# Kernel tuning notes

Measured on AMD Instinct MI355X. Metric: run time of the kernel, lower is better.

Reference implementation:

```python
import jax, jax.numpy as jnp
import numpy as np

DELTA_VAR = 0.5
DELTA_DIST = 1.5
VAR_WEIGHT = 1.0
DIST_WEIGHT = 1.0
REG_WEIGHT = 0.001
K = 16  # number of clusters (labels are in [0, K))


def setup_inputs() -> dict:
    key = jax.random.key(0)
    k1, k2 = jax.random.split(key)
    data = jax.random.normal(k1, (32, 512, 1024), dtype=jnp.float32)
    labels = jax.random.randint(k2, (512, 1024), 0, K, dtype=jnp.int32)
    return {"data": data, "labels": labels}


def reference(data, labels):
    D = data.shape[0]
    pts = data.reshape(D, -1).T          # [N, D] per-pixel embeddings
    lab = labels.reshape(-1)             # [N]

    # Per-cluster size and mean (center). All K clusters are present.
    counts = jax.ops.segment_sum(jnp.ones_like(lab, dtype=pts.dtype), lab,
                                 num_segments=K)          # [K]
    sums = jax.ops.segment_sum(pts, lab, num_segments=K)  # [K, D]
    centers = sums / counts[:, None]                      # [K, D]

    # Variance term: sum over all points of hinge(||center - x|| - dv)^2 / K
    diff = centers[lab] - pts                             # [N, D]
    dist = jnp.sqrt(jnp.sum(diff * diff, axis=-1))        # [N]
    var_term = jnp.sum(jnp.maximum(dist - DELTA_VAR, 0.0) ** 2) / K

    # Distance term: ordered pairs i != j of hinge(2*dd - ||ci - cj||)^2
    cd = centers[:, None, :] - centers[None, :, :]        # [K, K, D]
    sq = jnp.sum(cd * cd, axis=-1)                        # [K, K]
    eye = jnp.eye(K, dtype=bool)
    pd = jnp.sqrt(jnp.where(eye, 1.0, sq))                # safe sqrt on diag
    hinge = jnp.where(eye, 0.0, jnp.maximum(2.0 * DELTA_DIST - pd, 0.0) ** 2)
    dist_term = jnp.sum(hinge) / (K * (K - 1))

    # Regularization term: mean center norm
    reg_term = jnp.sum(jnp.sqrt(jnp.sum(centers * centers, axis=-1))) / K

    return VAR_WEIGHT * var_term + DIST_WEIGHT * dist_term + REG_WEIGHT * reg_term
```

## Files before the change

### kernel.cpp

```cpp
#include <hip/hip_runtime.h>


constexpr int KC = 16;
constexpr int DD = 32;
constexpr int NN = 512 * 1024;
constexpr int N4 = NN / 4;
constexpr int CHUNKS = 32;
constexpr int GROUPS_PER_CHUNK = N4 / CHUNKS;
constexpr int K1_ITERS = GROUPS_PER_CHUNK / 256;

constexpr int WS_SUMS = 0;
constexpr int WS_CNTS = 8192;
constexpr int WS_CT2  = 8448;
constexpr int WS_ZERO_FLOATS = 8448;

__global__ __launch_bounds__(256) void k1_sums(const float4* __restrict__ data4,
                                               const int4* __restrict__ lab4,
                                               float* __restrict__ ws) {
    const int tid = threadIdx.x;
    const int d = blockIdx.y;
    const bool doCnt = (d == 0);

    __shared__ float acc[256 * 17];
    __shared__ float cnt[256 * 17];
    float* arow = acc + tid * 17;
    float* crow = cnt + tid * 17;
#pragma unroll
    for (int k = 0; k < KC; ++k) arow[k] = 0.f;
    if (doCnt) {
#pragma unroll
        for (int k = 0; k < KC; ++k) crow[k] = 0.f;
    }

    const int base = blockIdx.x * GROUPS_PER_CHUNK + tid;
    const float4* dplane = data4 + (size_t)d * N4;

    for (int it = 0; it < K1_ITERS; ++it) {
        const int g = base + it * 256;
        const float4 v = dplane[g];
        const int4 lb = lab4[g];
        arow[lb.x] += v.x;
        arow[lb.y] += v.y;
        arow[lb.z] += v.z;
        arow[lb.w] += v.w;
        if (doCnt) {
            crow[lb.x] += 1.f;
            crow[lb.y] += 1.f;
            crow[lb.z] += 1.f;
            crow[lb.w] += 1.f;
        }
    }
    __syncthreads();

    const int k = tid >> 4, seg = tid & 15;
    float s = 0.f;
#pragma unroll
    for (int i = 0; i < 16; ++i) s += acc[(seg * 16 + i) * 17 + k];
#pragma unroll
    for (int off = 8; off > 0; off >>= 1) s += __shfl_down(s, off, 16);
    if (seg == 0) atomicAdd(&ws[WS_SUMS + (k * DD + d) * 16], s);
    if (doCnt) {
        float c = 0.f;
#pragma unroll
        for (int i = 0; i < 16; ++i) c += cnt[(seg * 16 + i) * 17 + k];
#pragma unroll
        for (int off = 8; off > 0; off >>= 1) c += __shfl_down(c, off, 16);
        if (seg == 0) atomicAdd(&ws[WS_CNTS + k * 16], c);
    }
}

__global__ __launch_bounds__(256) void k2_centers(float* __restrict__ ws,
                                                  float* __restrict__ out) {
    __shared__ float cent[KC][DD + 1];
    __shared__ float red[256];
    const int tid = threadIdx.x;

    for (int idx = tid; idx < KC * DD; idx += 256) {
        const int k = idx / DD, d = idx % DD;
        const float c = ws[WS_SUMS + idx * 16] / ws[WS_CNTS + k * 16];
        cent[k][d] = c;
        ws[WS_CT2 + d * 32 + k] = c;
        ws[WS_CT2 + d * 32 + 16 + k] = c;
    }
    __syncthreads();

    const int i = tid >> 4, j = tid & 15;
    float sq = 0.f;
#pragma unroll
    for (int d = 0; d < DD; ++d) {
        const float df = cent[i][d] - cent[j][d];
        sq += df * df;
    }
    float val = 0.f;
    if (i != j) {
        const float pd = sqrtf(sq);
        const float t = fmaxf(3.0f - pd, 0.f);
        val = t * t * (1.0f / (KC * (KC - 1)));
    } else {
        float s2 = 0.f;
#pragma unroll
        for (int d = 0; d < DD; ++d) s2 += cent[i][d] * cent[i][d];
        val = sqrtf(s2) * (0.001f / KC);
    }
    red[tid] = val;
    __syncthreads();
    for (int off = 128; off > 0; off >>= 1) {
        if (tid < off) red[tid] += red[tid + off];
        __syncthreads();
    }
    if (tid == 0) out[0] = red[0];
}

__global__ __launch_bounds__(256) void k3_var(const float4* __restrict__ data4,
                                              const int4* __restrict__ lab4,
                                              const float* __restrict__ ws,
                                              float* __restrict__ out) {
    __shared__ float ct2[DD * 32];
    const int tid = threadIdx.x;
    for (int idx = tid; idx < DD * 32; idx += 256) ct2[idx] = ws[WS_CT2 + idx];
    __syncthreads();

    const int g = blockIdx.x * 256 + tid;
    const int4 lb = lab4[g];
    const int dup = (tid & 32) >> 1;
    const int o0 = lb.x + dup, o1 = lb.y + dup, o2 = lb.z + dup, o3 = lb.w + dup;

    float s0 = 0.f, s1 = 0.f, s2 = 0.f, s3 = 0.f;
#pragma unroll 8
    for (int d = 0; d < DD; ++d) {
        const float4 v = data4[(size_t)d * N4 + g];
        const float* ctd = ct2 + d * 32;
        const float d0 = ctd[o0] - v.x; s0 += d0 * d0;
        const float d1 = ctd[o1] - v.y; s1 += d1 * d1;
        const float d2 = ctd[o2] - v.z; s2 += d2 * d2;
        const float d3 = ctd[o3] - v.w; s3 += d3 * d3;
    }
    const float h0 = fmaxf(sqrtf(s0) - 0.5f, 0.f);
    const float h1 = fmaxf(sqrtf(s1) - 0.5f, 0.f);
    const float h2 = fmaxf(sqrtf(s2) - 0.5f, 0.f);
    const float h3 = fmaxf(sqrtf(s3) - 0.5f, 0.f);
    float lsum = h0 * h0 + h1 * h1 + h2 * h2 + h3 * h3;

#pragma unroll
    for (int off = 32; off > 0; off >>= 1) lsum += __shfl_down(lsum, off);
    __shared__ float wred[4];
    if ((tid & 63) == 0) wred[tid >> 6] = lsum;
    __syncthreads();
    if (tid == 0) {
        const float s = wred[0] + wred[1] + wred[2] + wred[3];
        atomicAdd(out, s * (1.0f / KC));
    }
}

extern "C" void kernel_launch(void* const* d_in, const int* in_sizes, int n_in,
                              void* d_out, int out_size, void* d_ws, size_t ws_size,
                              hipStream_t stream) {
    const float4* data4 = (const float4*)d_in[0];
    const int4* lab4 = (const int4*)d_in[1];
    float* out = (float*)d_out;
    float* ws = (float*)d_ws;

    hipMemsetAsync(ws, 0, WS_ZERO_FLOATS * sizeof(float), stream);

    k1_sums<<<dim3(CHUNKS, DD), 256, 0, stream>>>(data4, lab4, ws);
    k2_centers<<<1, 256, 0, stream>>>(ws, out);
    k3_var<<<512, 256, 0, stream>>>(data4, lab4, ws, out);
}
```

Baseline: 122.0 us.

## Drop memset and center kernel by writing per-chunk partials and reducing redundantly

The sums kernel now writes per-chunk partial sums and counts to distinct workspace slots instead of using atomics, so the workspace memset is no longer needed. The separate single-block centers kernel is folded into the variance kernel: every block reduces the partials and computes the centers itself, and block 0 also adds the distance and regularization terms to the output. This cuts two stream operations and their launch gaps, at the cost of each of 512 blocks reading 16K partial floats from L2.

```diff
diff --git a/kernel.cpp b/kernel.cpp
--- a/kernel.cpp
+++ b/kernel.cpp
@@ -9,17 +9,19 @@
 constexpr int GROUPS_PER_CHUNK = N4 / CHUNKS;
 constexpr int K1_ITERS = GROUPS_PER_CHUNK / 256;
 
-constexpr int WS_SUMS = 0;
-constexpr int WS_CNTS = 8192;
-constexpr int WS_CT2  = 8448;
-constexpr int WS_ZERO_FLOATS = 8448;
+constexpr int WS_P  = 0;
+constexpr int WS_CP = 16384;
 
-__global__ __launch_bounds__(256) void k1_sums(const float4* __restrict__ data4,
+__global__ __launch_bounds__(256) void kA_sums(const float4* __restrict__ data4,
                                                const int4* __restrict__ lab4,
-                                               float* __restrict__ ws) {
+                                               float* __restrict__ ws,
+                                               float* __restrict__ out) {
     const int tid = threadIdx.x;
+    const int chunk = blockIdx.x;
     const int d = blockIdx.y;
     const bool doCnt = (d == 0);
+
+    if (chunk == 0 && d == 0 && tid == 0) out[0] = 0.f;
 
     __shared__ float acc[256 * 17];
     __shared__ float cnt[256 * 17];
@@ -32,7 +34,7 @@
         for (int k = 0; k < KC; ++k) crow[k] = 0.f;
     }
 
-    const int base = blockIdx.x * GROUPS_PER_CHUNK + tid;
+    const int base = chunk * GROUPS_PER_CHUNK + tid;
     const float4* dplane = data4 + (size_t)d * N4;
 
     for (int it = 0; it < K1_ITERS; ++it) {
@@ -58,67 +60,86 @@
     for (int i = 0; i < 16; ++i) s += acc[(seg * 16 + i) * 17 + k];
 #pragma unroll
     for (int off = 8; off > 0; off >>= 1) s += __shfl_down(s, off, 16);
-    if (seg == 0) atomicAdd(&ws[WS_SUMS + (k * DD + d) * 16], s);
+    if (seg == 0) ws[WS_P + (k * DD + d) * CHUNKS + chunk] = s;
     if (doCnt) {
         float c = 0.f;
 #pragma unroll
         for (int i = 0; i < 16; ++i) c += cnt[(seg * 16 + i) * 17 + k];
 #pragma unroll
         for (int off = 8; off > 0; off >>= 1) c += __shfl_down(c, off, 16);
-        if (seg == 0) atomicAdd(&ws[WS_CNTS + k * 16], c);
+        if (seg == 0) ws[WS_CP + k * CHUNKS + chunk] = c;
     }
 }
 
-__global__ __launch_bounds__(256) void k2_centers(float* __restrict__ ws,
-                                                  float* __restrict__ out) {
-    __shared__ float cent[KC][DD + 1];
-    __shared__ float red[256];
+__global__ __launch_bounds__(256) void kB_var(const float4* __restrict__ data4,
+                                              const int4* __restrict__ lab4,
+                                              const float* __restrict__ ws,
+                                              float* __restrict__ out) {
+    __shared__ float csum[KC * 33];
+    __shared__ float ccnt[KC];
+    __shared__ float ct2[DD * 32];
     const int tid = threadIdx.x;
 
-    for (int idx = tid; idx < KC * DD; idx += 256) {
-        const int k = idx / DD, d = idx % DD;
-        const float c = ws[WS_SUMS + idx * 16] / ws[WS_CNTS + k * 16];
-        cent[k][d] = c;
-        ws[WS_CT2 + d * 32 + k] = c;
-        ws[WS_CT2 + d * 32 + 16 + k] = c;
+    {
+        int idx = tid;
+        const float* p = ws + WS_P + idx * CHUNKS;
+        float s = 0.f;
+#pragma unroll
+        for (int c = 0; c < CHUNKS; ++c) s += p[c];
+        csum[(idx >> 5) * 33 + (idx & 31)] = s;
+        idx = tid + 256;
+        p = ws + WS_P + idx * CHUNKS;
+        s = 0.f;
+#pragma unroll
+        for (int c = 0; c < CHUNKS; ++c) s += p[c];
+        csum[(idx >> 5) * 33 + (idx & 31)] = s;
+    }
+    if (tid < KC) {
+        const float* p = ws + WS_CP + tid * CHUNKS;
+        float c = 0.f;
+#pragma unroll
+        for (int i = 0; i < CHUNKS; ++i) c += p[i];
+        ccnt[tid] = c;
     }
     __syncthreads();
 
-    const int i = tid >> 4, j = tid & 15;
-    float sq = 0.f;
+    for (int idx = tid; idx < KC * DD; idx += 256) {
+        const int k = idx >> 5, d = idx & 31;
+        const float c = csum[k * 33 + d] / ccnt[k];
+        ct2[d * 32 + k] = c;
+        ct2[d * 32 + 16 + k] = c;
+    }
+    __syncthreads();
+
+    if (blockIdx.x == 0) {
+        const int i = tid >> 4, j = tid & 15;
+        float val;
+        if (i != j) {
+            float sq = 0.f;
 #pragma unroll
-    for (int d = 0; d < DD; ++d) {
-        const float df = cent[i][d] - cent[j][d];
-        sq += df * df;
-    }
-    float val = 0.f;
-    if (i != j) {
-        const float pd = sqrtf(sq);
-        const float t = fmaxf(3.0f - pd, 0.f);
-        val = t * t * (1.0f / (KC * (KC - 1)));
-    } else {
-        float s2 = 0.f;
+            for (int d = 0; d < DD; ++d) {
+                const float df = ct2[d * 32 + i] - ct2[d * 32 + j];
+                sq += df * df;
+            }
+            const float pd = sqrtf(sq);
+            const float t = fmaxf(3.0f - pd, 0.f);
+            val = t * t * (1.0f / (KC * (KC - 1)));
+        } else {
+            float s2 = 0.f;
 #pragma unroll
-        for (int d = 0; d < DD; ++d) s2 += cent[i][d] * cent[i][d];
-        val = sqrtf(s2) * (0.001f / KC);
-    }
-    red[tid] = val;
-    __syncthreads();
-    for (int off = 128; off > 0; off >>= 1) {
-        if (tid < off) red[tid] += red[tid + off];
+            for (int d = 0; d < DD; ++d) s2 += ct2[d * 32 + i] * ct2[d * 32 + i];
+            val = sqrtf(s2) * (0.001f / KC);
+        }
+        __shared__ float red[256];
+        red[tid] = val;
+        __syncthreads();
+        for (int off = 128; off > 0; off >>= 1) {
+            if (tid < off) red[tid] += red[tid + off];
+            __syncthreads();
+        }
+        if (tid == 0) atomicAdd(out, red[0]);
         __syncthreads();
     }
-    if (tid == 0) out[0] = red[0];
-}
-
-__global__ __launch_bounds__(256) void k3_var(const float4* __restrict__ data4,
-                                              const int4* __restrict__ lab4,
-                                              const float* __restrict__ ws,
-                                              float* __restrict__ out) {
-    __shared__ float ct2[DD * 32];
-    const int tid = threadIdx.x;
-    for (int idx = tid; idx < DD * 32; idx += 256) ct2[idx] = ws[WS_CT2 + idx];
-    __syncthreads();
 
     const int g = blockIdx.x * 256 + tid;
     const int4 lb = lab4[g];
@@ -160,9 +181,6 @@
     float* out = (float*)d_out;
     float* ws = (float*)d_ws;
 
-    hipMemsetAsync(ws, 0, WS_ZERO_FLOATS * sizeof(float), stream);
-
-    k1_sums<<<dim3(CHUNKS, DD), 256, 0, stream>>>(data4, lab4, ws);
-    k2_centers<<<1, 256, 0, stream>>>(ws, out);
-    k3_var<<<512, 256, 0, stream>>>(data4, lab4, ws, out);
+    kA_sums<<<dim3(CHUNKS, DD), 256, 0, stream>>>(data4, lab4, ws, out);
+    kB_var<<<512, 256, 0, stream>>>(data4, lab4, ws, out);
 }
```

After: 119.0 us. 1.03x faster.
